# Kernel optimization log

Hardware: AMD Instinct MI355X
Metric: run time of the kernel (lower is better)

## Reference

```python
import jax, jax.numpy as jnp
import numpy as np

# Module hyperparameters (init_kwargs)
OSFREQ = 8.0      # oversampling_frequency
MAXFREQ = 1.0     # maximum_frequency
PERIOD = 1.0      # sampling_period
THRESH = 0.0      # thresh


def _periodogram_cfg(n_samples):
    """Angular frequencies and sample times for the oversampled periodogram."""
    timespan = PERIOD * (n_samples + 1) - 1
    all_samples = PERIOD * jnp.arange(1, n_samples + 1, dtype=jnp.float32)  # (T,)
    freqstep = 1.0 / (timespan * OSFREQ)
    n_freqs = int(np.floor((MAXFREQ * n_samples / (2.0 * timespan)) / freqstep))
    angular_frequencies = (2.0 * np.pi * freqstep) * jnp.arange(
        1, n_freqs + 1, dtype=jnp.float32
    )  # (F,)
    return angular_frequencies, all_samples


def _fit_spectrum(basis_masked, data_masked):
    """Least-squares projection of observed data onto each (masked) basis fn.
    basis_masked: (B, F, T) zeroed at unseen frames; data_masked: (B, C, T)."""
    num = jnp.einsum('bft,bct->bfc', basis_masked, data_masked)
    den = (basis_masked ** 2).sum(-1)[..., None]  # (B, F, 1)
    spectrum = num / den
    if THRESH > 0:
        a = jnp.abs(spectrum)
        spectrum = jnp.where(a / a.max() <= THRESH, 0.0, spectrum)
    return spectrum  # (B, F, C)


def _spectral_interpolate(data, mask):
    # data: (B, C, T) float; mask: (B, 1, T) bool (True = observed)
    B, C, T = data.shape
    w = mask.astype(data.dtype)          # (B, 1, T)
    wt = w[:, 0, :]                      # (B, T)
    ang, t = _periodogram_cfg(T)         # (F,), (T,)
    arg = ang[:, None] * t[None, :]      # (F, T)

    # Per-frequency phase offset tau from observed timepoints only (mask-weighted)
    num = jnp.einsum('bt,ft->bf', wt, jnp.sin(2.0 * arg))
    den = jnp.einsum('bt,ft->bf', wt, jnp.cos(2.0 * arg))
    tau = jnp.arctan2(num, den) / (2.0 * ang)              # (B, F)

    shifted = arg[None, :, :] - (ang[None, :] * tau)[..., None]  # (B, F, T)
    sin_basis = jnp.sin(shifted)
    cos_basis = jnp.cos(shifted)
    sin_m = sin_basis * wt[:, None, :]   # basis restricted to observed frames
    cos_m = cos_basis * wt[:, None, :]
    data_m = data * w

    sin_spec = _fit_spectrum(sin_m, data_m)  # (B, F, C)
    cos_spec = _fit_spectrum(cos_m, data_m)

    # Reconstruct the full time series from the fitted spectrum
    recon = (jnp.einsum('bft,bfc->bct', sin_basis, sin_spec)
             + jnp.einsum('bft,bfc->bct', cos_basis, cos_spec))  # (B, C, T)

    # Normalise: match per-channel std over observed frames (unbiased)
    n_obs = wt.sum(-1)[:, None]          # (B, 1)
    def wstd(x):
        m = (x * w).sum(-1) / n_obs                               # (B, C)
        v = (((x - m[..., None]) ** 2) * w).sum(-1) / (n_obs - 1)
        return jnp.sqrt(v)
    norm_fac = wstd(recon) / wstd(data)  # (B, C)
    recon = recon / norm_fac[..., None]

    # Keep observed samples, fill censored frames with the reconstruction
    return jnp.where(mask, data, recon)


def setup_inputs() -> dict:
    key = jax.random.key(0)
    k1, k2 = jax.random.split(key)
    data = jax.random.normal(k1, (4, 512, 1024), dtype=jnp.float32)
    mask = jax.random.bernoulli(k2, 0.75, (4, 1, 1024))  # True = observed
    return {"data": data, "mask": mask}


def reference(data, mask):
    return _spectral_interpolate(data, mask)
```

## Files before the change

kernel.cpp:

```cpp
#include <hip/hip_runtime.h>
#include <hip/hip_bf16.h>
#include <hip/hip_fp16.h>

using bf16 = __hip_bfloat16;
typedef __attribute__((ext_vector_type(8))) short bf16x8;
typedef __attribute__((ext_vector_type(4))) short short4v;
typedef __attribute__((ext_vector_type(2))) short short2v;
typedef __attribute__((ext_vector_type(4))) float f32x4;
typedef __attribute__((ext_vector_type(2))) _Float16 halfx2;

#define C_2PI_8192 7.6699039394282072e-4f

static __device__ __forceinline__ short bf16bits(float v) {
  bf16 h = __float2bfloat16(v);
  return *reinterpret_cast<short*>(&h);
}

#define GLOAD(gp, lp)                                                          \
  __builtin_amdgcn_global_load_lds(                                            \
      (const __attribute__((address_space(1))) void*)(gp),                     \
      (__attribute__((address_space(3))) void*)(lp), 16, 0, 0)

#define DETECT_BYTEMODE(mask, tid, outvar)                                     \
  __shared__ int _cnt;                                                         \
  if ((tid) == 0) _cnt = 0;                                                    \
  __syncthreads();                                                             \
  {                                                                            \
    const unsigned char* _mb = (const unsigned char*)(mask);                   \
    int _c = 0;                                                                \
    _Pragma("unroll")                                                          \
    for (int _i = 0; _i < 16; ++_i) _c += (_mb[(tid) * 16 + _i] != 0) ? 1 : 0; \
    atomicAdd(&_cnt, _c);                                                      \
  }                                                                            \
  __syncthreads();                                                             \
  const bool outvar = (_cnt > 2048);

static __device__ __forceinline__ float mask_w(const void* mask, bool bytemode, int e) {
  if (bytemode) return (((const unsigned char*)mask)[e] != 0) ? 1.f : 0.f;
  return (((const int*)mask)[e] != 0) ? 1.f : 0.f;
}

__global__ __launch_bounds__(256) void k_pre(const void* __restrict__ mask,
                                             const float* __restrict__ data,
                                             bf16* __restrict__ AE,
                                             bf16* __restrict__ Be,
                                             bf16* __restrict__ dmE,
                                             float4* __restrict__ scal,
                                             float* __restrict__ delta,
                                             float* __restrict__ invA) {
  int bid = blockIdx.x, tid = threadIdx.x;
  if (bid < 4096) {
    int region = bid >> 10;
    int idx = (bid & 1023) * 256 + tid;
    short4v lo, hi;
    if (region < 2) {
      int r = idx >> 6, j8 = (idx & 63) << 3;
      int m = (r & 2047) + 1;
      bool is_sin = (r < 2048);
      int ph0 = (region == 0) ? ((m * (2 * j8 + 2)) & 8191) : ((m * (2 * j8 + 1)) & 8191);
      int step = (2 * m) & 8191;
      float s = __sinf(ph0 * C_2PI_8192), c = __cosf(ph0 * C_2PI_8192);
      float sr = __sinf(step * C_2PI_8192), cr = __cosf(step * C_2PI_8192);
#pragma unroll
      for (int j = 0; j < 8; ++j) {
        float v = is_sin ? s : c;
        if (j < 4) lo[j] = bf16bits(v); else hi[j - 4] = bf16bits(v);
        float ns = s * cr + c * sr;
        c = c * cr - s * sr;
        s = ns;
      }
      short* dst = (short*)AE + (size_t)region * 2097152 + ((size_t)r << 9) + j8;
      *(short4v*)dst = lo;
      *(short4v*)(dst + 4) = hi;
    } else {
      int jr = idx >> 9, k8 = (idx & 511) << 3;
      int tau = (region == 2) ? (2 * jr + 2) : (2 * jr + 1);
      int m0 = (k8 & 2047) + 1;
      bool is_sin = (k8 < 2048);
      int ph0 = (m0 * tau) & 8191;
      float s = __sinf(ph0 * C_2PI_8192), c = __cosf(ph0 * C_2PI_8192);
      float sr = __sinf(tau * C_2PI_8192), cr = __cosf(tau * C_2PI_8192);
#pragma unroll
      for (int j = 0; j < 8; ++j) {
        float v = is_sin ? s : c;
        if (j < 4) lo[j] = bf16bits(v); else hi[j - 4] = bf16bits(v);
        float ns = s * cr + c * sr;
        c = c * cr - s * sr;
        s = ns;
      }
      short* dst = (short*)Be + (size_t)(region - 2) * 2097152 + ((size_t)jr << 12) + k8;
      *(short4v*)dst = lo;
      *(short4v*)(dst + 4) = hi;
    }
    return;
  }
  DETECT_BYTEMODE(mask, tid, bytemode)
  int wid = tid >> 6, lane = tid & 63;
  if (bid < 4100) {
    int b = bid - 4096;
    int base_b = b << 10;
    const float W = (float)(6.283185307179586 / 8192.0);
    const float ang = W * 4096.0f;
    __shared__ float red[4][2];
    __shared__ float bc2[2];
    float num = 0.f, den = 0.f;
    for (int t = tid; t < 1024; t += 256) {
      float arg = ang * (float)(t + 1);
      float w = mask_w(mask, bytemode, base_b + t);
      num += w * sinf(2.0f * arg);
      den += w * cosf(2.0f * arg);
    }
#pragma unroll
    for (int m = 32; m; m >>= 1) {
      num += __shfl_xor(num, m, 64);
      den += __shfl_xor(den, m, 64);
    }
    if (lane == 0) { red[wid][0] = num; red[wid][1] = den; }
    __syncthreads();
    if (tid == 0) {
      float a0 = red[0][0] + red[1][0] + red[2][0] + red[3][0];
      float a1 = red[0][1] + red[1][1] + red[2][1] + red[3][1];
      float tau = atan2f(a0, a1) / (2.0f * ang);
      bc2[0] = ang * tau;
    }
    __syncthreads();
    float P = bc2[0];
    float dss = 0.f;
    for (int t = tid; t < 1024; t += 256) {
      float arg = ang * (float)(t + 1);
      float d = sinf(arg - P);
      delta[base_b + t] = d;
      float w = mask_w(mask, bytemode, base_b + t);
      dss += w * d * d;
    }
#pragma unroll
    for (int m = 32; m; m >>= 1) dss += __shfl_xor(dss, m, 64);
    if (lane == 0) red[wid][0] = dss;
    __syncthreads();
    if (tid == 0)
      invA[b] = 1.f / (red[0][0] + red[1][0] + red[2][0] + red[3][0]);
  } else if (bid < 6148) {
    int gw = (bid - 4100) * 4 + wid;
    int b = gw >> 11, f = gw & 2047;
    int base_b = b << 10;
    float num = 0.f, den = 0.f, nb = 0.f;
    int f2 = 2 * (f + 1);
    {
      int ph0 = (f2 * (lane + 1)) & 8191;
      int st = (f2 << 6) & 8191;
      float s = __sinf(ph0 * C_2PI_8192), c = __cosf(ph0 * C_2PI_8192);
      float sr = __sinf(st * C_2PI_8192), cr = __cosf(st * C_2PI_8192);
#pragma unroll
      for (int i = 0; i < 16; ++i) {
        float w = mask_w(mask, bytemode, base_b + lane + (i << 6));
        num += w * s;
        den += w * c;
        nb += w;
        float ns = s * cr + c * sr;
        c = c * cr - s * sr;
        s = ns;
      }
    }
#pragma unroll
    for (int m = 32; m; m >>= 1) {
      num += __shfl_xor(num, m, 64);
      den += __shfl_xor(den, m, 64);
      nb += __shfl_xor(nb, m, 64);
    }
    if (lane == 0) {
      float th = 0.5f * atan2f(num, den);
      float c = cosf(th), s = sinf(th);
      float WSS = 0.5f * (nb - den);
      float WCC = 0.5f * (nb + den);
      float WSC = 0.5f * num;
      float den_s = c * c * WSS - 2.f * c * s * WSC + s * s * WCC;
      float den_c = c * c * WCC + 2.f * c * s * WSC + s * s * WSS;
      scal[gw] = make_float4(c, s, 1.f / den_s, 1.f / den_c);
    }
  } else {
    int bc = bid - 6148, b = bc >> 9;
    bf16* dmO = dmE + (1 << 20);
    size_t base = (size_t)bc * 1024 + tid * 4;
    float4 d4 = *(const float4*)(data + base);
    const float* d = (const float*)&d4;
    int me = (b << 10) + tid * 4;
    float wd[4];
#pragma unroll
    for (int j = 0; j < 4; ++j) wd[j] = mask_w(mask, bytemode, me + j) * d[j];
    short2v dE, dO;
    dO[0] = bf16bits(wd[0]); dE[0] = bf16bits(wd[1]);
    dO[1] = bf16bits(wd[2]); dE[1] = bf16bits(wd[3]);
    *(short2v*)((short*)dmE + (size_t)bc * 512 + tid * 2) = dE;
    *(short2v*)((short*)dmO + (size_t)bc * 512 + tid * 2) = dO;
  }
}

__global__ __launch_bounds__(512, 4) void k_gemm1_pq(const bf16* __restrict__ dmE,
                                                     const bf16* __restrict__ AE,
                                                     const float4* __restrict__ scal,
                                                     bf16* __restrict__ PQe,
                                                     bf16* __restrict__ PQo) {
  __shared__ bf16 As[128 * 64];
  __shared__ bf16 Bs[128 * 64];
  int bid = blockIdx.x;
  int swz = ((bid & 7) << 6) | (bid >> 3);
  int mt = swz & 15, ft = swz >> 4;
  int m0 = mt << 7, f0 = ft << 6;
  int tid = threadIdx.x, lane = tid & 63, wid = tid >> 6;
  int wm = (wid >> 2) << 6, wn = (wid & 3) << 5;
  int fr = lane & 15, kh = lane >> 4;

  int r0 = tid >> 3;
  int scol = ((tid & 7) ^ (r0 & 7)) << 3;
  const bf16* pa0 = dmE + (size_t)(m0 + r0) * 512 + scol;
  const bf16* pb0;
  const bf16* pb1;
  {
    int row0 = r0, row1 = 64 + r0;
    int g0 = ((row0 >> 4) & 1) * 2048 + f0 + (row0 & 15) + ((row0 >> 5) << 4);
    int g1 = ((row1 >> 4) & 1) * 2048 + f0 + (row1 & 15) + ((row1 >> 5) << 4);
    pb0 = AE + (size_t)g0 * 512 + scol;
    pb1 = AE + (size_t)g1 * 512 + scol;
  }
  char* lA = (char*)As + (wid << 10);
  char* lB = (char*)Bs + (wid << 10);

  f32x4 accU[4][2] = {};
  f32x4 accV[4][2] = {};
  int sw = fr & 7;

#define K_BODY(ACC)                                                              \
  for (int kt = 0; kt < 8; ++kt) {                                               \
    GLOAD(pa0, lA);                                                              \
    GLOAD(pa0 + 32768, lA + 8192);                                               \
    GLOAD(pb0, lB);                                                              \
    GLOAD(pb1, lB + 8192);                                                       \
    pa0 += 64; pb0 += 64; pb1 += 64;                                             \
    __syncthreads();                                                             \
    _Pragma("unroll")                                                            \
    for (int s = 0; s < 2; ++s) {                                                \
      bf16x8 a[4];                                                               \
      _Pragma("unroll")                                                          \
      for (int i = 0; i < 4; ++i)                                                \
        a[i] = *(const bf16x8*)&As[(wm + i * 16 + fr) * 64 + ((((s << 2) + kh) ^ sw) << 3)]; \
      _Pragma("unroll")                                                          \
      for (int j = 0; j < 2; ++j) {                                              \
        bf16x8 bb = *(const bf16x8*)&Bs[(wn + j * 16 + fr) * 64 + ((((s << 2) + kh) ^ sw) << 3)]; \
        _Pragma("unroll")                                                        \
        for (int i = 0; i < 4; ++i)                                              \
          ACC[i][j] = __builtin_amdgcn_mfma_f32_16x16x32_bf16(a[i], bb, ACC[i][j], 0, 0, 0); \
      }                                                                          \
    }                                                                            \
    __syncthreads();                                                             \
  }

  K_BODY(accU)
  pa0 += (1 << 20) - 512;
  pb0 += (2 << 20) - 512;
  pb1 += (2 << 20) - 512;
  K_BODY(accV)
#undef K_BODY

  int b = m0 >> 9;
  short* pqe = (short*)PQe;
  short* pqo = (short*)PQo;
  {
    int f = f0 + (wn >> 1) + fr;
    float4 sc = scal[(b << 11) + f];
    float c = sc.x, s = sc.y, ids = sc.z, idc = sc.w;
    bool self = (f == 2047);
#pragma unroll
    for (int i = 0; i < 4; ++i) {
#pragma unroll
      for (int q = 0; q < 4; ++q) {
        int bc = m0 + wm + i * 16 + (kh << 2) + q;
        float US = accU[i][0][q], UC = accU[i][1][q];
        float VS = accV[i][0][q], VC = accV[i][1][q];
        float Gs = US + VS, Gc = UC + VC;
        float gs = VS - US, gc = UC - VC;
        float ss = (c * Gs - s * Gc) * ids;
        float cs = (c * Gc + s * Gs) * idc;
        float P = c * ss + s * cs;
        float Q = c * cs - s * ss;
        float ssp = (c * gs + s * gc) * ids;
        float csp = (c * gc - s * gs) * idc;
        float Pp = self ? 0.f : (c * ssp - s * csp);
        float Qp = self ? 0.f : (c * csp + s * ssp);
        size_t base = (size_t)bc * 4096 + f;
        pqe[base] = bf16bits(P - Pp);
        pqe[base + 2048] = bf16bits(Q + Qp);
        pqo[base] = bf16bits(P + Pp);
        pqo[base + 2048] = bf16bits(Q - Qp);
      }
    }
  }
}

__global__ __launch_bounds__(512, 4) void k_gemm2(const bf16* __restrict__ PQe,
                                                  const bf16* __restrict__ Be,
                                                  _Float16* __restrict__ Pe) {
  __shared__ bf16 As[128 * 64];
  __shared__ bf16 Bs[128 * 64];
  int bid = blockIdx.x;
  int swz = ((bid & 7) << 6) | (bid >> 3);
  int eo = swz >> 8;
  int slice = (swz >> 6) & 3;
  int tl = swz & 63;
  int mt = tl & 15, nt = tl >> 4;
  int m0 = mt << 7, n0 = nt << 7;
  int tid = threadIdx.x, lane = tid & 63, wid = tid >> 6;
  int wm = (wid >> 2) << 6, wn = (wid & 3) << 5;
  int fr = lane & 15, kh = lane >> 4;

  const bf16* A = PQe + (size_t)eo * (8 << 20);
  const bf16* B = Be + (size_t)eo * (2 << 20);
  _Float16* C = Pe + (size_t)eo * (8 << 20);

  int r0 = tid >> 3;
  int scol = ((tid & 7) ^ (r0 & 7)) << 3;
  const bf16* pa0 = A + (size_t)slice * 1024 + (size_t)(m0 + r0) * 4096 + scol;
  const bf16* pb0 = B + (size_t)slice * 1024 + (size_t)(n0 + r0) * 4096 + scol;
  _Float16* Cp = C + (size_t)slice * 1048576;
  char* lA = (char*)As + (wid << 10);
  char* lB = (char*)Bs + (wid << 10);

  f32x4 acc[4][2] = {};
  int sw = fr & 7;

  for (int kt = 0; kt < 16; ++kt) {
    GLOAD(pa0, lA);
    GLOAD(pa0 + 262144, lA + 8192);
    GLOAD(pb0, lB);
    GLOAD(pb0 + 262144, lB + 8192);
    pa0 += 64; pb0 += 64;
    __syncthreads();
#pragma unroll
    for (int s = 0; s < 2; ++s) {
      bf16x8 a[4];
#pragma unroll
      for (int i = 0; i < 4; ++i)
        a[i] = *(const bf16x8*)&As[(wm + i * 16 + fr) * 64 + ((((s << 2) + kh) ^ sw) << 3)];
#pragma unroll
      for (int j = 0; j < 2; ++j) {
        bf16x8 bb = *(const bf16x8*)&Bs[(wn + j * 16 + fr) * 64 + ((((s << 2) + kh) ^ sw) << 3)];
#pragma unroll
        for (int i = 0; i < 4; ++i)
          acc[i][j] = __builtin_amdgcn_mfma_f32_16x16x32_bf16(a[i], bb, acc[i][j], 0, 0, 0);
      }
    }
    __syncthreads();
  }
#pragma unroll
  for (int i = 0; i < 4; ++i) {
#pragma unroll
    for (int q = 0; q < 4; ++q) {
      size_t row = m0 + wm + i * 16 + (kh << 2) + q;
      _Float16* cp = Cp + row * 512 + n0 + wn + fr;
#pragma unroll
      for (int j = 0; j < 2; ++j) cp[j * 16] = (_Float16)acc[i][j][q];
    }
  }
}

__global__ __launch_bounds__(256) void k_tail(const _Float16* __restrict__ Pe,
                                              const _Float16* __restrict__ Po,
                                              const float* __restrict__ data,
                                              const void* __restrict__ mask,
                                              const float* __restrict__ delta,
                                              const float* __restrict__ invA,
                                              float* __restrict__ out) {
  int bc = blockIdx.x, b = bc >> 9, tid = threadIdx.x;
  DETECT_BYTEMODE(mask, tid, bytemode)
  int wid = tid >> 6, lane = tid & 63;
  size_t base = (size_t)bc * 1024 + tid * 4;
  int jj = tid * 2;
  float r[4] = {0.f, 0.f, 0.f, 0.f};
#pragma unroll
  for (int s = 0; s < 4; ++s) {
    halfx2 pe = *(const halfx2*)(Pe + (size_t)s * 1048576 + (size_t)bc * 512 + jj);
    halfx2 po = *(const halfx2*)(Po + (size_t)s * 1048576 + (size_t)bc * 512 + jj);
    r[0] += (float)po[0];
    r[1] += (float)pe[0];
    r[2] += (float)po[1];
    r[3] += (float)pe[1];
  }
  float4 e4 = *(const float4*)(delta + (b << 10) + tid * 4);
  float4 d4 = *(const float4*)(data + base);
  const float* e = (const float*)&e4;
  const float* d = (const float*)&d4;
  float w[4];
  int me = (b << 10) + tid * 4;
#pragma unroll
  for (int j = 0; j < 4; ++j) w[j] = mask_w(mask, bytemode, me + j);
  float nbv = 0.f, sd = 0.f, sd2 = 0.f, sdd = 0.f, sdc = 0.f;
#pragma unroll
  for (int j = 0; j < 4; ++j) {
    float wd = w[j] * d[j];
    nbv += w[j];
    sd += wd;
    sd2 += wd * d[j];
    sdd += wd * e[j];
    sdc += (j & 1) ? wd : -wd;
  }
#pragma unroll
  for (int m = 32; m; m >>= 1) {
    nbv += __shfl_xor(nbv, m, 64);
    sd += __shfl_xor(sd, m, 64);
    sd2 += __shfl_xor(sd2, m, 64);
    sdd += __shfl_xor(sdd, m, 64);
    sdc += __shfl_xor(sdc, m, 64);
  }
  __shared__ float red[4][5];
  __shared__ float bcast[3];
  if (lane == 0) {
    red[wid][0] = nbv; red[wid][1] = sd; red[wid][2] = sd2;
    red[wid][3] = sdd; red[wid][4] = sdc;
  }
  __syncthreads();
  if (tid == 0) {
    float n = red[0][0] + red[1][0] + red[2][0] + red[3][0];
    float a1 = red[0][1] + red[1][1] + red[2][1] + red[3][1];
    float a2 = red[0][2] + red[1][2] + red[2][2] + red[3][2];
    float a3 = red[0][3] + red[1][3] + red[2][3] + red[3][3];
    float a4 = red[0][4] + red[1][4] + red[2][4] + red[3][4];
    bcast[0] = a3 * invA[b];
    bcast[1] = a4 / n;
    float md = a1 / n;
    bcast[2] = (a2 - n * md * md) / (n - 1.f);
    red[0][0] = n;
  }
  __syncthreads();
  float ssv = bcast[0], csv = bcast[1];
  float sr = 0.f, sr2 = 0.f;
#pragma unroll
  for (int j = 0; j < 4; ++j) {
    r[j] += e[j] * ssv + ((j & 1) ? csv : -csv);
    float wr = w[j] * r[j];
    sr += wr;
    sr2 += wr * r[j];
  }
#pragma unroll
  for (int m = 32; m; m >>= 1) {
    sr += __shfl_xor(sr, m, 64);
    sr2 += __shfl_xor(sr2, m, 64);
  }
  __shared__ float red2[4][2];
  __shared__ float s_inv;
  if (lane == 0) { red2[wid][0] = sr; red2[wid][1] = sr2; }
  __syncthreads();
  if (tid == 0) {
    float a0 = red2[0][0] + red2[1][0] + red2[2][0] + red2[3][0];
    float a1 = red2[0][1] + red2[1][1] + red2[2][1] + red2[3][1];
    float n = red[0][0];
    float mr = a0 / n, vr = (a1 - n * mr * mr) / (n - 1.f);
    s_inv = sqrtf(bcast[2] / vr);
  }
  __syncthreads();
  float inv = s_inv;
  float4 o;
  ((float*)&o)[0] = (w[0] != 0.f) ? d[0] : r[0] * inv;
  ((float*)&o)[1] = (w[1] != 0.f) ? d[1] : r[1] * inv;
  ((float*)&o)[2] = (w[2] != 0.f) ? d[2] : r[2] * inv;
  ((float*)&o)[3] = (w[3] != 0.f) ? d[3] : r[3] * inv;
  *(float4*)(out + base) = o;
}

extern "C" void kernel_launch(void* const* d_in, const int* in_sizes, int n_in,
                              void* d_out, int out_size, void* d_ws, size_t ws_size,
                              hipStream_t stream) {
  const float* data = (const float*)d_in[0];
  const void* mask = d_in[1];
  float* out = (float*)d_out;
  char* ws = (char*)d_ws;

  float* invA = (float*)(ws + 16640);
  float* delta = (float*)(ws + 50176);
  float4* scal = (float4*)(ws + 131072);
  const size_t MB = 1ull << 20;
  bf16* AE = (bf16*)(ws + 1 * MB);
  bf16* Be = (bf16*)(ws + 9 * MB);
  bf16* dmE = (bf16*)(ws + 17 * MB);
  bf16* PQe = (bf16*)(ws + 21 * MB);
  bf16* PQo = (bf16*)(ws + 37 * MB);
  _Float16* Pe = (_Float16*)(ws + 53 * MB);
  _Float16* Po = (_Float16*)(ws + 69 * MB);

  k_pre<<<8196, 256, 0, stream>>>(mask, data, AE, Be, dmE, scal, delta, invA);
  k_gemm1_pq<<<512, 512, 0, stream>>>(dmE, AE, scal, PQe, PQo);
  k_gemm2<<<512, 512, 0, stream>>>(PQe, Be, Pe);
  k_tail<<<2048, 256, 0, stream>>>(Pe, Po, data, mask, delta, invA, out);
}
```

Measured before the change: 87.60 us.

## Decompose time axis into residue classes to shrink analysis and synthesis GEMMs

Restructures the DFT-like projection by splitting the time index into 4-way residue classes. This gives a smaller analysis GEMM (K=256) and a smaller synthesis GEMM (K=2048, N=256). Per-frequency phase rotations are applied in the GEMM epilogue, and a few special frequencies are handled in closed form in the tail kernel. The aim is to cut basis-table generation and total GEMM work and traffic, at the cost of more complex epilogue arithmetic and more bf16 rounding paths.

```diff
diff --git a/kernel.cpp b/kernel.cpp
--- a/kernel.cpp
+++ b/kernel.cpp
@@ -7,7 +7,6 @@
 typedef __attribute__((ext_vector_type(4))) short short4v;
 typedef __attribute__((ext_vector_type(2))) short short2v;
 typedef __attribute__((ext_vector_type(4))) float f32x4;
-typedef __attribute__((ext_vector_type(2))) _Float16 halfx2;
 
 #define C_2PI_8192 7.6699039394282072e-4f
 
@@ -42,105 +41,57 @@
 
 __global__ __launch_bounds__(256) void k_pre(const void* __restrict__ mask,
                                              const float* __restrict__ data,
-                                             bf16* __restrict__ AE,
-                                             bf16* __restrict__ Be,
-                                             bf16* __restrict__ dmE,
+                                             bf16* __restrict__ B_ana,
+                                             bf16* __restrict__ B_syn,
+                                             bf16* __restrict__ A_ana,
                                              float4* __restrict__ scal,
                                              float* __restrict__ delta,
                                              float* __restrict__ invA) {
   int bid = blockIdx.x, tid = threadIdx.x;
-  if (bid < 4096) {
-    int region = bid >> 10;
-    int idx = (bid & 1023) * 256 + tid;
+  if (bid < 256) {
+    int row = (bid << 3) + (tid >> 5);
+    int u8 = (tid & 31) << 3;
+    int Mt = ((row >> 5) << 4) | (row & 15);
+    bool is_cos = (row >> 4) & 1;
+    int step = (4 * Mt) & 8191;
+    int ph = (4 * Mt * u8) & 8191;
     short4v lo, hi;
-    if (region < 2) {
-      int r = idx >> 6, j8 = (idx & 63) << 3;
-      int m = (r & 2047) + 1;
-      bool is_sin = (r < 2048);
-      int ph0 = (region == 0) ? ((m * (2 * j8 + 2)) & 8191) : ((m * (2 * j8 + 1)) & 8191);
-      int step = (2 * m) & 8191;
-      float s = __sinf(ph0 * C_2PI_8192), c = __cosf(ph0 * C_2PI_8192);
-      float sr = __sinf(step * C_2PI_8192), cr = __cosf(step * C_2PI_8192);
-#pragma unroll
-      for (int j = 0; j < 8; ++j) {
-        float v = is_sin ? s : c;
-        if (j < 4) lo[j] = bf16bits(v); else hi[j - 4] = bf16bits(v);
-        float ns = s * cr + c * sr;
-        c = c * cr - s * sr;
-        s = ns;
-      }
-      short* dst = (short*)AE + (size_t)region * 2097152 + ((size_t)r << 9) + j8;
-      *(short4v*)dst = lo;
-      *(short4v*)(dst + 4) = hi;
-    } else {
-      int jr = idx >> 9, k8 = (idx & 511) << 3;
-      int tau = (region == 2) ? (2 * jr + 2) : (2 * jr + 1);
-      int m0 = (k8 & 2047) + 1;
-      bool is_sin = (k8 < 2048);
-      int ph0 = (m0 * tau) & 8191;
-      float s = __sinf(ph0 * C_2PI_8192), c = __cosf(ph0 * C_2PI_8192);
-      float sr = __sinf(tau * C_2PI_8192), cr = __cosf(tau * C_2PI_8192);
-#pragma unroll
-      for (int j = 0; j < 8; ++j) {
-        float v = is_sin ? s : c;
-        if (j < 4) lo[j] = bf16bits(v); else hi[j - 4] = bf16bits(v);
-        float ns = s * cr + c * sr;
-        c = c * cr - s * sr;
-        s = ns;
-      }
-      short* dst = (short*)Be + (size_t)(region - 2) * 2097152 + ((size_t)jr << 12) + k8;
-      *(short4v*)dst = lo;
-      *(short4v*)(dst + 4) = hi;
-    }
+#pragma unroll
+    for (int j = 0; j < 8; ++j) {
+      float x = ph * C_2PI_8192;
+      float v = is_cos ? __cosf(x) : __sinf(x);
+      if (j < 4) lo[j] = bf16bits(v); else hi[j - 4] = bf16bits(v);
+      ph = (ph + step) & 8191;
+    }
+    short* dst = (short*)B_ana + (size_t)row * 256 + u8;
+    *(short4v*)dst = lo;
+    *(short4v*)(dst + 4) = hi;
+    return;
+  }
+  if (bid < 512) {
+    int u = bid - 256;
+    int m0 = tid << 2;
+    int step = (4 * u) & 8191;
+    int ph = (4 * u * m0) & 8191;
+    short4v lo, hi;
+#pragma unroll
+    for (int i = 0; i < 4; ++i) {
+      float x = ph * C_2PI_8192;
+      short sv = bf16bits(__sinf(x));
+      short cv = bf16bits(__cosf(x));
+      if (i < 2) { lo[2 * i] = sv; lo[2 * i + 1] = cv; }
+      else { hi[2 * (i - 2)] = sv; hi[2 * (i - 2) + 1] = cv; }
+      ph = (ph + step) & 8191;
+    }
+    short* dst = (short*)B_syn + (size_t)u * 2048 + (m0 << 1);
+    *(short4v*)dst = lo;
+    *(short4v*)(dst + 4) = hi;
     return;
   }
   DETECT_BYTEMODE(mask, tid, bytemode)
   int wid = tid >> 6, lane = tid & 63;
-  if (bid < 4100) {
-    int b = bid - 4096;
-    int base_b = b << 10;
-    const float W = (float)(6.283185307179586 / 8192.0);
-    const float ang = W * 4096.0f;
-    __shared__ float red[4][2];
-    __shared__ float bc2[2];
-    float num = 0.f, den = 0.f;
-    for (int t = tid; t < 1024; t += 256) {
-      float arg = ang * (float)(t + 1);
-      float w = mask_w(mask, bytemode, base_b + t);
-      num += w * sinf(2.0f * arg);
-      den += w * cosf(2.0f * arg);
-    }
-#pragma unroll
-    for (int m = 32; m; m >>= 1) {
-      num += __shfl_xor(num, m, 64);
-      den += __shfl_xor(den, m, 64);
-    }
-    if (lane == 0) { red[wid][0] = num; red[wid][1] = den; }
-    __syncthreads();
-    if (tid == 0) {
-      float a0 = red[0][0] + red[1][0] + red[2][0] + red[3][0];
-      float a1 = red[0][1] + red[1][1] + red[2][1] + red[3][1];
-      float tau = atan2f(a0, a1) / (2.0f * ang);
-      bc2[0] = ang * tau;
-    }
-    __syncthreads();
-    float P = bc2[0];
-    float dss = 0.f;
-    for (int t = tid; t < 1024; t += 256) {
-      float arg = ang * (float)(t + 1);
-      float d = sinf(arg - P);
-      delta[base_b + t] = d;
-      float w = mask_w(mask, bytemode, base_b + t);
-      dss += w * d * d;
-    }
-#pragma unroll
-    for (int m = 32; m; m >>= 1) dss += __shfl_xor(dss, m, 64);
-    if (lane == 0) red[wid][0] = dss;
-    __syncthreads();
-    if (tid == 0)
-      invA[b] = 1.f / (red[0][0] + red[1][0] + red[2][0] + red[3][0]);
-  } else if (bid < 6148) {
-    int gw = (bid - 4100) * 4 + wid;
+  if (bid < 2560) {
+    int gw = (bid - 512) * 4 + wid;
     int b = gw >> 11, f = gw & 2047;
     int base_b = b << 10;
     float num = 0.f, den = 0.f, nb = 0.f;
@@ -177,161 +128,218 @@
       float den_c = c * c * WCC + 2.f * c * s * WSC + s * s * WSS;
       scal[gw] = make_float4(c, s, 1.f / den_s, 1.f / den_c);
     }
+  } else if (bid < 2564) {
+    int b = bid - 2560;
+    int base_b = b << 10;
+    const float W = (float)(6.283185307179586 / 8192.0);
+    const float ang = W * 4096.0f;
+    __shared__ float red[4][2];
+    __shared__ float bc2[1];
+    float num = 0.f, den = 0.f;
+    for (int t = tid; t < 1024; t += 256) {
+      float arg = ang * (float)(t + 1);
+      float w = mask_w(mask, bytemode, base_b + t);
+      num += w * sinf(2.0f * arg);
+      den += w * cosf(2.0f * arg);
+    }
+#pragma unroll
+    for (int m = 32; m; m >>= 1) {
+      num += __shfl_xor(num, m, 64);
+      den += __shfl_xor(den, m, 64);
+    }
+    if (lane == 0) { red[wid][0] = num; red[wid][1] = den; }
+    __syncthreads();
+    if (tid == 0) {
+      float a0 = red[0][0] + red[1][0] + red[2][0] + red[3][0];
+      float a1 = red[0][1] + red[1][1] + red[2][1] + red[3][1];
+      float tau = atan2f(a0, a1) / (2.0f * ang);
+      bc2[0] = ang * tau;
+    }
+    __syncthreads();
+    float P = bc2[0];
+    float dss = 0.f;
+    for (int t = tid; t < 1024; t += 256) {
+      float arg = ang * (float)(t + 1);
+      float d = sinf(arg - P);
+      delta[base_b + t] = d;
+      float w = mask_w(mask, bytemode, base_b + t);
+      dss += w * d * d;
+    }
+#pragma unroll
+    for (int m = 32; m; m >>= 1) dss += __shfl_xor(dss, m, 64);
+    if (lane == 0) red[wid][0] = dss;
+    __syncthreads();
+    if (tid == 0)
+      invA[b] = 1.f / (red[0][0] + red[1][0] + red[2][0] + red[3][0]);
   } else {
-    int bc = bid - 6148, b = bc >> 9;
-    bf16* dmO = dmE + (1 << 20);
+    int bc = bid - 2564, b = bc >> 9;
     size_t base = (size_t)bc * 1024 + tid * 4;
     float4 d4 = *(const float4*)(data + base);
     const float* d = (const float*)&d4;
     int me = (b << 10) + tid * 4;
-    float wd[4];
-#pragma unroll
-    for (int j = 0; j < 4; ++j) wd[j] = mask_w(mask, bytemode, me + j) * d[j];
-    short2v dE, dO;
-    dO[0] = bf16bits(wd[0]); dE[0] = bf16bits(wd[1]);
-    dO[1] = bf16bits(wd[2]); dE[1] = bf16bits(wd[3]);
-    *(short2v*)((short*)dmE + (size_t)bc * 512 + tid * 2) = dE;
-    *(short2v*)((short*)dmO + (size_t)bc * 512 + tid * 2) = dO;
-  }
-}
-
-__global__ __launch_bounds__(512, 4) void k_gemm1_pq(const bf16* __restrict__ dmE,
-                                                     const bf16* __restrict__ AE,
+    short* A = (short*)A_ana;
+#pragma unroll
+    for (int j = 0; j < 4; ++j) {
+      float wd = mask_w(mask, bytemode, me + j) * d[j];
+      A[(size_t)((bc << 2) + j) * 256 + tid] = bf16bits(wd);
+    }
+  }
+}
+
+__global__ __launch_bounds__(512, 4) void k_gemm_ana(const bf16* __restrict__ A_ana,
+                                                     const bf16* __restrict__ B_ana,
                                                      const float4* __restrict__ scal,
-                                                     bf16* __restrict__ PQe,
-                                                     bf16* __restrict__ PQo) {
+                                                     bf16* __restrict__ A_syn) {
+  __shared__ bf16 As[128 * 64];
+  __shared__ bf16 Bs[128 * 64];
+  int bid = blockIdx.x;
+  int swz = ((bid & 7) << 7) | (bid >> 3);
+  int mt = swz & 63, nt = swz >> 6;
+  int m0 = mt << 7, n0 = nt << 7;
+  int tid = threadIdx.x, lane = tid & 63, wid = tid >> 6;
+  int wm = (wid >> 2) << 6, wn = (wid & 3) << 5;
+  int fr = lane & 15, kh = lane >> 4;
+
+  int r0 = tid >> 3;
+  int scol = ((tid & 7) ^ (r0 & 7)) << 3;
+  const bf16* pa0 = A_ana + (size_t)(m0 + r0) * 256 + scol;
+  const bf16* pb0 = B_ana + (size_t)(n0 + r0) * 256 + scol;
+  char* lA = (char*)As + (wid << 10);
+  char* lB = (char*)Bs + (wid << 10);
+
+  f32x4 acc[4][2] = {};
+  int sw = fr & 7;
+
+  for (int kt = 0; kt < 4; ++kt) {
+    GLOAD(pa0, lA);
+    GLOAD(pa0 + 16384, lA + 8192);
+    GLOAD(pb0, lB);
+    GLOAD(pb0 + 16384, lB + 8192);
+    pa0 += 64; pb0 += 64;
+    __syncthreads();
+#pragma unroll
+    for (int s = 0; s < 2; ++s) {
+      bf16x8 a[4];
+#pragma unroll
+      for (int i = 0; i < 4; ++i)
+        a[i] = *(const bf16x8*)&As[(wm + i * 16 + fr) * 64 + ((((s << 2) + kh) ^ sw) << 3)];
+#pragma unroll
+      for (int j = 0; j < 2; ++j) {
+        bf16x8 bb = *(const bf16x8*)&Bs[(wn + j * 16 + fr) * 64 + ((((s << 2) + kh) ^ sw) << 3)];
+#pragma unroll
+        for (int i = 0; i < 4; ++i)
+          acc[i][j] = __builtin_amdgcn_mfma_f32_16x16x32_bf16(a[i], bb, acc[i][j], 0, 0, 0);
+      }
+    }
+    __syncthreads();
+  }
+
+  int mt_ = ((n0 + wn) >> 1) + fr;
+  short* Asn = (short*)A_syn;
+  if (mt_ == 0) {
+#pragma unroll
+    for (int i = 0; i < 4; ++i) {
+      int bc = (m0 + wm + i * 16 + (kh << 2)) >> 2;
+#pragma unroll
+      for (int r = 0; r < 4; ++r) {
+        short2v z; z[0] = 0; z[1] = 0;
+        *(short2v*)&Asn[(size_t)((r << 11) + bc) * 2048] = z;
+      }
+    }
+    return;
+  }
+  float a1 = mt_ * C_2PI_8192;
+  float s1, c1;
+  __sincosf(a1, &s1, &c1);
+  float c2 = c1 * c1 - s1 * s1, s2 = 2.f * c1 * s1;
+  float c4 = c2 * c2 - s2 * s2, s4 = 2.f * c2 * s2;
+  int b = m0 >> 11;
+  float4 scA = scal[(b << 11) + mt_ - 1];
+  float4 scB = scal[(b << 11) + 2047 - mt_];
+  const float sig[4] = {1.f, -1.f, 1.f, -1.f};
+  const float c1m[4] = {c1, s1, -s1, -c1}, s1m[4] = {s1, c1, c1, s1};
+  const float c2m[4] = {c2, -c2, -c2, c2}, s2m[4] = {s2, s2, -s2, -s2};
+  const float s4m[4] = {s4, -s4, s4, -s4};
+  const float cm[4] = {scA.x, scB.x, scB.x, scA.x};
+  const float sm[4] = {scA.y, scB.y, -scB.y, -scA.y};
+  const float ids[4] = {scA.z, scB.z, scB.z, scA.z};
+  const float idc[4] = {scA.w, scB.w, scB.w, scA.w};
+#pragma unroll
+  for (int i = 0; i < 4; ++i) {
+    int bc = (m0 + wm + i * 16 + (kh << 2)) >> 2;
+    f32x4 S = acc[i][0], C = acc[i][1];
+    float PrF[4] = {0.f, 0.f, 0.f, 0.f};
+    float QrF[4] = {0.f, 0.f, 0.f, 0.f};
+#pragma unroll
+    for (int t = 0; t < 4; ++t) {
+      float ES = sig[t] * S[3], EC = C[3];
+      float UE_S = c4 * ES + s4m[t] * EC;
+      float UE_C = c4 * EC - s4m[t] * ES;
+      float OS = sig[t] * S[1], OC = C[1];
+      float U_S = UE_S + c2m[t] * OS + s2m[t] * OC;
+      float U_C = UE_C + c2m[t] * OC - s2m[t] * OS;
+      float PS = sig[t] * S[0], PC = C[0];
+      float WS = sig[t] * S[2], WC = C[2];
+      float VpS = PS + c2m[t] * WS + s2m[t] * WC;
+      float VpC = PC + c2m[t] * WC - s2m[t] * WS;
+      float V_S = c1m[t] * VpS + s1m[t] * VpC;
+      float V_C = c1m[t] * VpC - s1m[t] * VpS;
+      float GS = U_S + V_S, GC = U_C + V_C;
+      float ss = (cm[t] * GS - sm[t] * GC) * ids[t];
+      float cs = (cm[t] * GC + sm[t] * GS) * idc[t];
+      float P = cm[t] * ss + sm[t] * cs;
+      float Q = cm[t] * cs - sm[t] * ss;
+      float cr3 = c1m[t] * c2m[t] - s1m[t] * s2m[t];
+      float sr3 = s1m[t] * c2m[t] + c1m[t] * s2m[t];
+      const float cr[4] = {c1m[t], c2m[t], cr3, c4};
+      const float sr_[4] = {s1m[t], s2m[t], sr3, s4m[t]};
+#pragma unroll
+      for (int r = 0; r < 4; ++r) {
+        PrF[r] += sig[t] * (P * cr[r] - Q * sr_[r]);
+        QrF[r] += P * sr_[r] + Q * cr[r];
+      }
+    }
+#pragma unroll
+    for (int r = 0; r < 4; ++r) {
+      short2v v;
+      v[0] = bf16bits(PrF[r]);
+      v[1] = bf16bits(QrF[r]);
+      *(short2v*)&Asn[(size_t)((r << 11) + bc) * 2048 + 2 * mt_] = v;
+    }
+  }
+}
+
+__global__ __launch_bounds__(512, 4) void k_gemm_syn(const bf16* __restrict__ A_syn,
+                                                     const bf16* __restrict__ B_syn,
+                                                     _Float16* __restrict__ Pe) {
   __shared__ bf16 As[128 * 64];
   __shared__ bf16 Bs[128 * 64];
   int bid = blockIdx.x;
   int swz = ((bid & 7) << 6) | (bid >> 3);
-  int mt = swz & 15, ft = swz >> 4;
-  int m0 = mt << 7, f0 = ft << 6;
-  int tid = threadIdx.x, lane = tid & 63, wid = tid >> 6;
-  int wm = (wid >> 2) << 6, wn = (wid & 3) << 5;
-  int fr = lane & 15, kh = lane >> 4;
-
-  int r0 = tid >> 3;
-  int scol = ((tid & 7) ^ (r0 & 7)) << 3;
-  const bf16* pa0 = dmE + (size_t)(m0 + r0) * 512 + scol;
-  const bf16* pb0;
-  const bf16* pb1;
-  {
-    int row0 = r0, row1 = 64 + r0;
-    int g0 = ((row0 >> 4) & 1) * 2048 + f0 + (row0 & 15) + ((row0 >> 5) << 4);
-    int g1 = ((row1 >> 4) & 1) * 2048 + f0 + (row1 & 15) + ((row1 >> 5) << 4);
-    pb0 = AE + (size_t)g0 * 512 + scol;
-    pb1 = AE + (size_t)g1 * 512 + scol;
-  }
-  char* lA = (char*)As + (wid << 10);
-  char* lB = (char*)Bs + (wid << 10);
-
-  f32x4 accU[4][2] = {};
-  f32x4 accV[4][2] = {};
-  int sw = fr & 7;
-
-#define K_BODY(ACC)                                                              \
-  for (int kt = 0; kt < 8; ++kt) {                                               \
-    GLOAD(pa0, lA);                                                              \
-    GLOAD(pa0 + 32768, lA + 8192);                                               \
-    GLOAD(pb0, lB);                                                              \
-    GLOAD(pb1, lB + 8192);                                                       \
-    pa0 += 64; pb0 += 64; pb1 += 64;                                             \
-    __syncthreads();                                                             \
-    _Pragma("unroll")                                                            \
-    for (int s = 0; s < 2; ++s) {                                                \
-      bf16x8 a[4];                                                               \
-      _Pragma("unroll")                                                          \
-      for (int i = 0; i < 4; ++i)                                                \
-        a[i] = *(const bf16x8*)&As[(wm + i * 16 + fr) * 64 + ((((s << 2) + kh) ^ sw) << 3)]; \
-      _Pragma("unroll")                                                          \
-      for (int j = 0; j < 2; ++j) {                                              \
-        bf16x8 bb = *(const bf16x8*)&Bs[(wn + j * 16 + fr) * 64 + ((((s << 2) + kh) ^ sw) << 3)]; \
-        _Pragma("unroll")                                                        \
-        for (int i = 0; i < 4; ++i)                                              \
-          ACC[i][j] = __builtin_amdgcn_mfma_f32_16x16x32_bf16(a[i], bb, ACC[i][j], 0, 0, 0); \
-      }                                                                          \
-    }                                                                            \
-    __syncthreads();                                                             \
-  }
-
-  K_BODY(accU)
-  pa0 += (1 << 20) - 512;
-  pb0 += (2 << 20) - 512;
-  pb1 += (2 << 20) - 512;
-  K_BODY(accV)
-#undef K_BODY
-
-  int b = m0 >> 9;
-  short* pqe = (short*)PQe;
-  short* pqo = (short*)PQo;
-  {
-    int f = f0 + (wn >> 1) + fr;
-    float4 sc = scal[(b << 11) + f];
-    float c = sc.x, s = sc.y, ids = sc.z, idc = sc.w;
-    bool self = (f == 2047);
-#pragma unroll
-    for (int i = 0; i < 4; ++i) {
-#pragma unroll
-      for (int q = 0; q < 4; ++q) {
-        int bc = m0 + wm + i * 16 + (kh << 2) + q;
-        float US = accU[i][0][q], UC = accU[i][1][q];
-        float VS = accV[i][0][q], VC = accV[i][1][q];
-        float Gs = US + VS, Gc = UC + VC;
-        float gs = VS - US, gc = UC - VC;
-        float ss = (c * Gs - s * Gc) * ids;
-        float cs = (c * Gc + s * Gs) * idc;
-        float P = c * ss + s * cs;
-        float Q = c * cs - s * ss;
-        float ssp = (c * gs + s * gc) * ids;
-        float csp = (c * gc - s * gs) * idc;
-        float Pp = self ? 0.f : (c * ssp - s * csp);
-        float Qp = self ? 0.f : (c * csp + s * ssp);
-        size_t base = (size_t)bc * 4096 + f;
-        pqe[base] = bf16bits(P - Pp);
-        pqe[base + 2048] = bf16bits(Q + Qp);
-        pqo[base] = bf16bits(P + Pp);
-        pqo[base + 2048] = bf16bits(Q - Qp);
-      }
-    }
-  }
-}
-
-__global__ __launch_bounds__(512, 4) void k_gemm2(const bf16* __restrict__ PQe,
-                                                  const bf16* __restrict__ Be,
-                                                  _Float16* __restrict__ Pe) {
-  __shared__ bf16 As[128 * 64];
-  __shared__ bf16 Bs[128 * 64];
-  int bid = blockIdx.x;
-  int swz = ((bid & 7) << 6) | (bid >> 3);
-  int eo = swz >> 8;
-  int slice = (swz >> 6) & 3;
-  int tl = swz & 63;
-  int mt = tl & 15, nt = tl >> 4;
+  int slice = swz >> 7;
+  int tl = swz & 127;
+  int mt = tl & 63, nt = tl >> 6;
   int m0 = mt << 7, n0 = nt << 7;
   int tid = threadIdx.x, lane = tid & 63, wid = tid >> 6;
   int wm = (wid >> 2) << 6, wn = (wid & 3) << 5;
   int fr = lane & 15, kh = lane >> 4;
 
-  const bf16* A = PQe + (size_t)eo * (8 << 20);
-  const bf16* B = Be + (size_t)eo * (2 << 20);
-  _Float16* C = Pe + (size_t)eo * (8 << 20);
-
   int r0 = tid >> 3;
   int scol = ((tid & 7) ^ (r0 & 7)) << 3;
-  const bf16* pa0 = A + (size_t)slice * 1024 + (size_t)(m0 + r0) * 4096 + scol;
-  const bf16* pb0 = B + (size_t)slice * 1024 + (size_t)(n0 + r0) * 4096 + scol;
-  _Float16* Cp = C + (size_t)slice * 1048576;
+  const bf16* pa0 = A_syn + (size_t)slice * 512 + (size_t)(m0 + r0) * 2048 + scol;
+  const bf16* pb0 = B_syn + (size_t)slice * 512 + (size_t)(n0 + r0) * 2048 + scol;
+  _Float16* Cp = Pe + (size_t)slice * 2097152;
   char* lA = (char*)As + (wid << 10);
   char* lB = (char*)Bs + (wid << 10);
 
   f32x4 acc[4][2] = {};
   int sw = fr & 7;
 
-  for (int kt = 0; kt < 16; ++kt) {
+  for (int kt = 0; kt < 8; ++kt) {
     GLOAD(pa0, lA);
-    GLOAD(pa0 + 262144, lA + 8192);
+    GLOAD(pa0 + 131072, lA + 8192);
     GLOAD(pb0, lB);
-    GLOAD(pb0 + 262144, lB + 8192);
+    GLOAD(pb0 + 131072, lB + 8192);
     pa0 += 64; pb0 += 64;
     __syncthreads();
 #pragma unroll
@@ -355,7 +363,7 @@
 #pragma unroll
     for (int q = 0; q < 4; ++q) {
       size_t row = m0 + wm + i * 16 + (kh << 2) + q;
-      _Float16* cp = Cp + row * 512 + n0 + wn + fr;
+      _Float16* cp = Cp + row * 256 + n0 + wn + fr;
 #pragma unroll
       for (int j = 0; j < 2; ++j) cp[j * 16] = (_Float16)acc[i][j][q];
     }
@@ -363,27 +371,29 @@
 }
 
 __global__ __launch_bounds__(256) void k_tail(const _Float16* __restrict__ Pe,
-                                              const _Float16* __restrict__ Po,
                                               const float* __restrict__ data,
                                               const void* __restrict__ mask,
                                               const float* __restrict__ delta,
                                               const float* __restrict__ invA,
+                                              const float4* __restrict__ scal,
                                               float* __restrict__ out) {
   int bc = blockIdx.x, b = bc >> 9, tid = threadIdx.x;
+  __shared__ float spat[8];
+  if (tid < 8) spat[tid] = __sinf(tid * 0.7853981633974483f);
   DETECT_BYTEMODE(mask, tid, bytemode)
   int wid = tid >> 6, lane = tid & 63;
   size_t base = (size_t)bc * 1024 + tid * 4;
-  int jj = tid * 2;
-  float r[4] = {0.f, 0.f, 0.f, 0.f};
-#pragma unroll
-  for (int s = 0; s < 4; ++s) {
-    halfx2 pe = *(const halfx2*)(Pe + (size_t)s * 1048576 + (size_t)bc * 512 + jj);
-    halfx2 po = *(const halfx2*)(Po + (size_t)s * 1048576 + (size_t)bc * 512 + jj);
-    r[0] += (float)po[0];
-    r[1] += (float)pe[0];
-    r[2] += (float)po[1];
-    r[3] += (float)pe[1];
-  }
+
+  float r[4];
+#pragma unroll
+  for (int j = 0; j < 4; ++j) {
+    size_t off = (size_t)((j << 11) + bc) * 256 + tid;
+    float a = 0.f;
+#pragma unroll
+    for (int s = 0; s < 4; ++s) a += (float)Pe[(size_t)s * 2097152 + off];
+    r[j] = a;
+  }
+
   float4 e4 = *(const float4*)(delta + (b << 10) + tid * 4);
   float4 d4 = *(const float4*)(data + base);
   const float* e = (const float*)&e4;
@@ -392,7 +402,9 @@
   int me = (b << 10) + tid * 4;
 #pragma unroll
   for (int j = 0; j < 4; ++j) w[j] = mask_w(mask, bytemode, me + j);
+
   float nbv = 0.f, sd = 0.f, sd2 = 0.f, sdd = 0.f, sdc = 0.f;
+  float gs1 = 0.f, gc1 = 0.f, gs2 = 0.f, gc2 = 0.f, gs3 = 0.f, gc3 = 0.f;
 #pragma unroll
   for (int j = 0; j < 4; ++j) {
     float wd = w[j] * d[j];
@@ -401,6 +413,11 @@
     sd2 += wd * d[j];
     sdd += wd * e[j];
     sdc += (j & 1) ? wd : -wd;
+    int tau = (tid << 2) + j + 1;
+    int i1 = tau & 7, i2 = (tau << 1) & 7, i3 = (tau * 3) & 7;
+    gs1 += wd * spat[i1]; gc1 += wd * spat[(i1 + 2) & 7];
+    gs2 += wd * spat[i2]; gc2 += wd * spat[(i2 + 2) & 7];
+    gs3 += wd * spat[i3]; gc3 += wd * spat[(i3 + 2) & 7];
   }
 #pragma unroll
   for (int m = 32; m; m >>= 1) {
@@ -409,32 +426,62 @@
     sd2 += __shfl_xor(sd2, m, 64);
     sdd += __shfl_xor(sdd, m, 64);
     sdc += __shfl_xor(sdc, m, 64);
-  }
-  __shared__ float red[4][5];
-  __shared__ float bcast[3];
+    gs1 += __shfl_xor(gs1, m, 64);
+    gc1 += __shfl_xor(gc1, m, 64);
+    gs2 += __shfl_xor(gs2, m, 64);
+    gc2 += __shfl_xor(gc2, m, 64);
+    gs3 += __shfl_xor(gs3, m, 64);
+    gc3 += __shfl_xor(gc3, m, 64);
+  }
+  __shared__ float red[4][11];
+  __shared__ float bcast[10];
   if (lane == 0) {
-    red[wid][0] = nbv; red[wid][1] = sd; red[wid][2] = sd2;
-    red[wid][3] = sdd; red[wid][4] = sdc;
+    float* rp = red[wid];
+    rp[0] = nbv; rp[1] = sd; rp[2] = sd2; rp[3] = sdd; rp[4] = sdc;
+    rp[5] = gs1; rp[6] = gc1; rp[7] = gs2; rp[8] = gc2; rp[9] = gs3; rp[10] = gc3;
   }
   __syncthreads();
   if (tid == 0) {
-    float n = red[0][0] + red[1][0] + red[2][0] + red[3][0];
-    float a1 = red[0][1] + red[1][1] + red[2][1] + red[3][1];
-    float a2 = red[0][2] + red[1][2] + red[2][2] + red[3][2];
-    float a3 = red[0][3] + red[1][3] + red[2][3] + red[3][3];
-    float a4 = red[0][4] + red[1][4] + red[2][4] + red[3][4];
-    bcast[0] = a3 * invA[b];
-    bcast[1] = a4 / n;
-    float md = a1 / n;
-    bcast[2] = (a2 - n * md * md) / (n - 1.f);
-    red[0][0] = n;
+    float a[11];
+#pragma unroll
+    for (int k = 0; k < 11; ++k) a[k] = red[0][k] + red[1][k] + red[2][k] + red[3][k];
+    float n = a[0];
+    bcast[0] = a[3] * invA[b];
+    bcast[1] = a[4] / n;
+    float md = a[1] / n;
+    bcast[2] = (a[2] - n * md * md) / (n - 1.f);
+    bcast[9] = n;
+    float4 s1v = scal[(b << 11) + 1023];
+    float c = s1v.x, s = s1v.y, is_ = s1v.z, ic_ = s1v.w;
+    float ss = (c * a[5] - s * a[6]) * is_;
+    float cs = (c * a[6] + s * a[5]) * ic_;
+    bcast[3] = c * ss + s * cs;
+    bcast[4] = c * cs - s * ss;
+    float ssp = (c * a[9] + s * a[10]) * is_;
+    float csp = (c * a[10] - s * a[9]) * ic_;
+    bcast[7] = c * ssp - s * csp;
+    bcast[8] = c * csp + s * ssp;
+    float4 s2v = scal[(b << 11) + 2047];
+    float c2 = s2v.x, s2 = s2v.y;
+    float ss2 = (c2 * a[7] - s2 * a[8]) * s2v.z;
+    float cs2 = (c2 * a[8] + s2 * a[7]) * s2v.w;
+    bcast[5] = c2 * ss2 + s2 * cs2;
+    bcast[6] = c2 * cs2 - s2 * ss2;
   }
   __syncthreads();
   float ssv = bcast[0], csv = bcast[1];
+  float P1 = bcast[3], Q1 = bcast[4], P2 = bcast[5], Q2 = bcast[6];
+  float P3 = bcast[7], Q3 = bcast[8];
+
   float sr = 0.f, sr2 = 0.f;
 #pragma unroll
   for (int j = 0; j < 4; ++j) {
-    r[j] += e[j] * ssv + ((j & 1) ? csv : -csv);
+    int tau = (tid << 2) + j + 1;
+    int i1 = tau & 7, i2 = (tau << 1) & 7, i3 = (tau * 3) & 7;
+    r[j] += e[j] * ssv + ((j & 1) ? csv : -csv)
+          + P1 * spat[i1] + Q1 * spat[(i1 + 2) & 7]
+          + P2 * spat[i2] + Q2 * spat[(i2 + 2) & 7]
+          + P3 * spat[i3] + Q3 * spat[(i3 + 2) & 7];
     float wr = w[j] * r[j];
     sr += wr;
     sr2 += wr * r[j];
@@ -451,7 +498,7 @@
   if (tid == 0) {
     float a0 = red2[0][0] + red2[1][0] + red2[2][0] + red2[3][0];
     float a1 = red2[0][1] + red2[1][1] + red2[2][1] + red2[3][1];
-    float n = red[0][0];
+    float n = bcast[9];
     float mr = a0 / n, vr = (a1 - n * mr * mr) / (n - 1.f);
     s_inv = sqrtf(bcast[2] / vr);
   }
@@ -477,16 +524,14 @@
   float* delta = (float*)(ws + 50176);
   float4* scal = (float4*)(ws + 131072);
   const size_t MB = 1ull << 20;
-  bf16* AE = (bf16*)(ws + 1 * MB);
-  bf16* Be = (bf16*)(ws + 9 * MB);
-  bf16* dmE = (bf16*)(ws + 17 * MB);
-  bf16* PQe = (bf16*)(ws + 21 * MB);
-  bf16* PQo = (bf16*)(ws + 37 * MB);
-  _Float16* Pe = (_Float16*)(ws + 53 * MB);
-  _Float16* Po = (_Float16*)(ws + 69 * MB);
-
-  k_pre<<<8196, 256, 0, stream>>>(mask, data, AE, Be, dmE, scal, delta, invA);
-  k_gemm1_pq<<<512, 512, 0, stream>>>(dmE, AE, scal, PQe, PQo);
-  k_gemm2<<<512, 512, 0, stream>>>(PQe, Be, Pe);
-  k_tail<<<2048, 256, 0, stream>>>(Pe, Po, data, mask, delta, invA, out);
-}
+  bf16* B_ana = (bf16*)(ws + 1 * MB);
+  bf16* B_syn = (bf16*)(ws + 2 * MB);
+  bf16* A_ana = (bf16*)(ws + 3 * MB);
+  bf16* A_syn = (bf16*)(ws + 8 * MB);
+  _Float16* Pe = (_Float16*)(ws + 41 * MB);
+
+  k_pre<<<4612, 256, 0, stream>>>(mask, data, B_ana, B_syn, A_ana, scal, delta, invA);
+  k_gemm_ana<<<1024, 512, 0, stream>>>(A_ana, B_ana, scal, A_syn);
+  k_gemm_syn<<<512, 512, 0, stream>>>(A_syn, B_syn, Pe);
+  k_tail<<<2048, 256, 0, stream>>>(Pe, data, mask, delta, invA, scal, out);
+}
```

Result: no change. 88.74 us (+1.3%).
